# Kernel optimization log

Hardware: AMD Instinct MI355X
Metric: run time of the kernel (lower is better)

Reference implementation:

```python
import jax, jax.numpy as jnp
import numpy as np

HID = 1024
HEADS = 16
HEAD_DIM = HID // HEADS
MLP_HID = 4096
TEMB = 1024
EPS = 1e-6


def _ln(x):
    # LayerNorm without affine, eps=1e-6
    mu = jnp.mean(x, axis=-1, keepdims=True)
    var = jnp.var(x, axis=-1, keepdims=True)
    return (x - mu) * jax.lax.rsqrt(var + EPS)


def _modulate(x, shift, scale):
    return x * (1.0 + scale[:, None, :]) + shift[:, None, :]


def setup_inputs() -> dict:
    key = jax.random.key(0)
    ks = jax.random.split(key, 12)
    s = 0.02
    return {
        "x": jax.random.normal(ks[0], (8, 1024, HID), jnp.float32),
        "c": jax.random.normal(ks[1], (8, TEMB), jnp.float32),
        "W_qkv": jax.random.normal(ks[2], (HID, 3 * HID), jnp.float32) * s,
        "b_qkv": jnp.zeros((3 * HID,), jnp.float32),
        "W_proj": jax.random.normal(ks[3], (HID, HID), jnp.float32) * s,
        "b_proj": jnp.zeros((HID,), jnp.float32),
        "W_fc1": jax.random.normal(ks[4], (HID, MLP_HID), jnp.float32) * s,
        "b_fc1": jnp.zeros((MLP_HID,), jnp.float32),
        "W_fc2": jax.random.normal(ks[5], (MLP_HID, HID), jnp.float32) * s,
        "b_fc2": jnp.zeros((HID,), jnp.float32),
        "W_ada": jax.random.normal(ks[6], (TEMB, 6 * HID), jnp.float32) * s,
        "b_ada": jnp.zeros((6 * HID,), jnp.float32),
    }


def _attn(x, W_qkv, b_qkv, W_proj, b_proj):
    B, N, C = x.shape
    qkv = x @ W_qkv + b_qkv                      # [B,N,3C]
    qkv = qkv.reshape(B, N, 3, HEADS, HEAD_DIM)
    q, k, v = qkv[:, :, 0], qkv[:, :, 1], qkv[:, :, 2]  # [B,N,H,D]
    scale = HEAD_DIM ** -0.5
    logits = jnp.einsum('bnhd,bmhd->bhnm', q, k) * scale
    attn = jax.nn.softmax(logits, axis=-1)
    out = jnp.einsum('bhnm,bmhd->bnhd', attn, v).reshape(B, N, C)
    return out @ W_proj + b_proj


def reference(x, c, W_qkv, b_qkv, W_proj, b_proj, W_fc1, b_fc1, W_fc2, b_fc2, W_ada, b_ada):
    ada = jax.nn.silu(c) @ W_ada + b_ada          # [B,6C]
    shift_msa, scale_msa, gate_msa, shift_mlp, scale_mlp, gate_mlp = jnp.split(ada, 6, axis=1)

    h = _modulate(_ln(x), shift_msa, scale_msa)
    x = x + gate_msa[:, None, :] * _attn(h, W_qkv, b_qkv, W_proj, b_proj)

    h = _modulate(_ln(x), shift_mlp, scale_mlp)
    h = jax.nn.gelu(h @ W_fc1 + b_fc1, approximate=True) @ W_fc2 + b_fc2
    x = x + gate_mlp[:, None, :] * h
    return x
```

## Files before the change

### kernel.cpp

```cpp
#include <hip/hip_runtime.h>
#include <stdint.h>

typedef unsigned short u16;
typedef __attribute__((ext_vector_type(4))) float f32x4;
typedef __attribute__((ext_vector_type(8))) short bf16x8;
typedef bf16x8 bf16x8a __attribute__((may_alias));
typedef uint32_t u32a __attribute__((may_alias));

#define HID 1024
#define MLPD 4096
#define TEMB 1024
#define ADA_N 6144
#define SEQ 1024
#define BATCH 8
#define KCH 32
#define KCHLEN (TEMB / KCH)

__device__ __forceinline__ u16 f2bf_bits(float f) {
  uint32_t u = __float_as_uint(f);
  uint32_t r = (u + 0x7FFFu + ((u >> 16) & 1u)) >> 16;
  return (u16)r;
}

__device__ __forceinline__ float bf2f(u16 b) {
  return __uint_as_float(((uint32_t)b) << 16);
}

__device__ __forceinline__ uint32_t cvt_pk_bf16(float lo, float hi) {
  uint32_t r;
  asm("v_cvt_pk_bf16_f32 %0, %1, %2" : "=v"(r) : "v"(lo), "v"(hi));
  return r;
}

__device__ __forceinline__ float exp2_hw(float x) {
#if __has_builtin(__builtin_amdgcn_exp2f)
  return __builtin_amdgcn_exp2f(x);
#else
  return exp2f(x);
#endif
}

__device__ __forceinline__ void async_copy16(void* lds_dst, const void* g_src) {
  __builtin_amdgcn_global_load_lds(
      (const __attribute__((address_space(1))) void*)(uintptr_t)g_src,
      (__attribute__((address_space(3))) void*)(uint32_t)(uintptr_t)lds_dst,
      16, 0, 0);
}

__device__ __forceinline__ float gelu_tanh(float v) {
  float u = 0.7978845608028654f * (v + 0.044715f * v * v * v);
  float e = __expf(2.f * u);
  return v * e / (e + 1.f);
}

__global__ __launch_bounds__(256) void transpose_bf16(const float* __restrict__ W,
                                                      u16* __restrict__ Wt, int K, int N) {
  __shared__ float tile[32][33];
  int n0 = blockIdx.x * 32, k0 = blockIdx.y * 32;
  int tx = threadIdx.x & 31, ty = threadIdx.x >> 5;
#pragma unroll
  for (int i = 0; i < 4; i++)
    tile[ty + i * 8][tx] = W[(size_t)(k0 + ty + i * 8) * N + n0 + tx];
  __syncthreads();
#pragma unroll
  for (int i = 0; i < 4; i++)
    Wt[(size_t)(n0 + ty + i * 8) * K + k0 + tx] = f2bf_bits(tile[tx][ty + i * 8]);
}

__global__ __launch_bounds__(256) void ada_part(const float* __restrict__ c,
                                                const float* __restrict__ W,
                                                float* __restrict__ part) {
  __shared__ float sc[BATCH * KCHLEN];
  int t = threadIdx.x;
  int col = blockIdx.x * 256 + t;
  int kc = blockIdx.y;
  int k0 = kc * KCHLEN;
  for (int i = t; i < BATCH * KCHLEN; i += 256) {
    int b = i >> 5, kk = i & (KCHLEN - 1);
    float v = c[b * TEMB + k0 + kk];
    sc[i] = v / (1.f + __expf(-v));
  }
  __syncthreads();
  float acc[BATCH] = {};
  for (int kk = 0; kk < KCHLEN; kk++) {
    float w = W[(size_t)(k0 + kk) * ADA_N + col];
#pragma unroll
    for (int b = 0; b < BATCH; b++) acc[b] += sc[b * KCHLEN + kk] * w;
  }
#pragma unroll
  for (int b = 0; b < BATCH; b++)
    part[((size_t)kc * BATCH + b) * ADA_N + col] = acc[b];
}

__global__ __launch_bounds__(256) void ada_reduce(const float* __restrict__ part,
                                                  const float* __restrict__ bias,
                                                  float* __restrict__ out) {
  int i = blockIdx.x * 256 + threadIdx.x;
  int col = i % ADA_N, b = i / ADA_N;
  float s = bias[col];
#pragma unroll
  for (int kc = 0; kc < KCH; kc++)
    s += part[((size_t)kc * BATCH + b) * ADA_N + col];
  out[(size_t)b * ADA_N + col] = s;
}

__global__ __launch_bounds__(256) void ln_mod(const float* __restrict__ x,
                                              const float* __restrict__ ada,
                                              int shift_off, int scale_off,
                                              u16* __restrict__ h) {
  int row = blockIdx.x;
  int bb = row >> 10;
  int t = threadIdx.x;
  const float4 v = ((const float4*)(x + (size_t)row * HID))[t];
  float s = v.x + v.y + v.z + v.w;
  float sq = v.x * v.x + v.y * v.y + v.z * v.z + v.w * v.w;
#pragma unroll
  for (int off = 32; off >= 1; off >>= 1) {
    s += __shfl_xor(s, off);
    sq += __shfl_xor(sq, off);
  }
  __shared__ float red[8];
  int wid = t >> 6;
  if ((t & 63) == 0) { red[wid] = s; red[4 + wid] = sq; }
  __syncthreads();
  s = red[0] + red[1] + red[2] + red[3];
  sq = red[4] + red[5] + red[6] + red[7];
  float mu = s * (1.0f / HID);
  float rs = rsqrtf(sq * (1.0f / HID) - mu * mu + 1e-6f);
  const float4 sc = ((const float4*)(ada + (size_t)bb * ADA_N + scale_off))[t];
  const float4 sh = ((const float4*)(ada + (size_t)bb * ADA_N + shift_off))[t];
  ushort4 o;
  o.x = f2bf_bits((v.x - mu) * rs * (1.f + sc.x) + sh.x);
  o.y = f2bf_bits((v.y - mu) * rs * (1.f + sc.y) + sh.y);
  o.z = f2bf_bits((v.z - mu) * rs * (1.f + sc.z) + sh.z);
  o.w = f2bf_bits((v.w - mu) * rs * (1.f + sc.w) + sh.w);
  ((ushort4*)(h + (size_t)row * HID))[t] = o;
}


template <int NLOAD>
__device__ __forceinline__ void stage_tile(u16* dst, const u16* gsrc, int K, int koff, int t) {
#pragma unroll
  for (int i = 0; i < NLOAD; ++i) {
    int slot = i * 512 + t;
    int row = slot >> 3, cp = slot & 7;
    const u16* src = gsrc + (size_t)row * K + koff + ((cp ^ (row & 7)) << 3);
    async_copy16(dst + slot * 8, src);
  }
}

#define LDSRD(buf, row, kk) \
  (*(const bf16x8a*)&(buf)[(row) * 64 + ((((kk) * 4 + l4) ^ ((row) & 7)) << 3)])

template <int EPI>
__global__ __launch_bounds__(512, 2) void gemm8(const u16* __restrict__ A,
                                                const u16* __restrict__ Bt,
                                                const float* __restrict__ bias,
                                                void* __restrict__ Cout,
                                                const float* __restrict__ resid,
                                                const float* __restrict__ gate,
                                                int N, int K) {
  __shared__ u16 lds[49152];
  u16* const As0 = lds;
  u16* const As1 = lds + 16384;
  u16* const Bs0 = lds + 32768;
  u16* const Bs1 = lds + 40960;

  int t = threadIdx.x;
  int lane = t & 63, wid = t >> 6;
  int l15 = lane & 15, l4 = lane >> 4;
  int wr = wid >> 2, wc = wid & 3;
  int lid = blockIdx.x;
  int xcd = lid & 7, win = lid >> 3;
  int m0 = (xcd * 4 + (win & 3)) * 256;
  int n0 = (win >> 2) * 128;

  const u16* Abase = A + (size_t)m0 * K;
  const u16* Bbase = Bt + (size_t)n0 * K;
  f32x4 acc[8][2] = {};

  stage_tile<4>(As0, Abase, K, 0, t);
  stage_tile<2>(Bs0, Bbase, K, 0, t);
  stage_tile<4>(As1, Abase, K, 64, t);
  stage_tile<2>(Bs1, Bbase, K, 64, t);
  int nt = K / 64;
  for (int ts = 0; ts < nt; ++ts) {
    u16* cA = (ts & 1) ? As1 : As0;
    u16* cB = (ts & 1) ? Bs1 : Bs0;
    if (ts == nt - 1) asm volatile("s_waitcnt vmcnt(0)" ::: "memory");
    else              asm volatile("s_waitcnt vmcnt(6)" ::: "memory");
    __builtin_amdgcn_s_barrier();
    asm volatile("" ::: "memory");
    bf16x8 bf[2][2], af[8][2];
#pragma unroll
    for (int ni = 0; ni < 2; ++ni)
#pragma unroll
      for (int kk = 0; kk < 2; ++kk)
        bf[ni][kk] = LDSRD(cB, wc * 32 + ni * 16 + l15, kk);
#pragma unroll
    for (int mi = 0; mi < 8; ++mi)
#pragma unroll
      for (int kk = 0; kk < 2; ++kk)
        af[mi][kk] = LDSRD(cA, wr * 128 + mi * 16 + l15, kk);
    asm volatile("s_waitcnt lgkmcnt(0)" ::: "memory");
    __builtin_amdgcn_s_barrier();
    if (ts + 2 < nt) {
      stage_tile<4>(cA, Abase, K, (ts + 2) * 64, t);
      stage_tile<2>(cB, Bbase, K, (ts + 2) * 64, t);
    }
    __builtin_amdgcn_s_setprio(1);
#pragma unroll
    for (int mi = 0; mi < 8; ++mi)
#pragma unroll
      for (int ni = 0; ni < 2; ++ni) {
        acc[mi][ni] = __builtin_amdgcn_mfma_f32_16x16x32_bf16(af[mi][0], bf[ni][0], acc[mi][ni], 0, 0, 0);
        acc[mi][ni] = __builtin_amdgcn_mfma_f32_16x16x32_bf16(af[mi][1], bf[ni][1], acc[mi][ni], 0, 0, 0);
      }
    __builtin_amdgcn_s_setprio(0);
  }

  const int EST = 132;
  int bb = m0 >> 10;
#pragma unroll
  for (int ni = 0; ni < 2; ++ni) {
    int col = wc * 32 + ni * 16 + l15;
    float bv = bias[n0 + col];
    float gv = (EPI == 2) ? gate[(size_t)bb * ADA_N + n0 + col] : 0.f;
#pragma unroll
    for (int mi = 0; mi < 8; ++mi)
#pragma unroll
      for (int r = 0; r < 4; ++r) {
        int row = wr * 128 + mi * 16 + l4 * 4 + r;
        float v = acc[mi][ni][r] + bv;
        if (EPI == 1) v = gelu_tanh(v);
        if (EPI == 2) v = gv * v;
        lds[row * EST + col] = f2bf_bits(v);
      }
  }
  asm volatile("s_waitcnt lgkmcnt(0)" ::: "memory");
  __builtin_amdgcn_s_barrier();
  asm volatile("" ::: "memory");
  {
    int row = t >> 1, half = t & 1;
    size_t grow = (size_t)(m0 + row) * N + n0 + half * 64;
#pragma unroll
    for (int j = 0; j < 8; ++j) {
      bf16x8 v = *(const bf16x8a*)&lds[row * EST + half * 64 + j * 8];
      if (EPI == 2) {
        const float4* rp = (const float4*)&resid[grow + j * 8];
        float4 o0 = rp[0], o1 = rp[1];
        o0.x += bf2f((u16)v[0]); o0.y += bf2f((u16)v[1]);
        o0.z += bf2f((u16)v[2]); o0.w += bf2f((u16)v[3]);
        o1.x += bf2f((u16)v[4]); o1.y += bf2f((u16)v[5]);
        o1.z += bf2f((u16)v[6]); o1.w += bf2f((u16)v[7]);
        float4* op = (float4*)((float*)Cout + grow + j * 8);
        op[0] = o0; op[1] = o1;
      } else {
        *(bf16x8a*)((u16*)Cout + grow + j * 8) = v;
      }
    }
  }
}

__global__ __launch_bounds__(256, 3) void attn_kernel(const u16* __restrict__ qkv,
                                                      u16* __restrict__ O) {
  const int KSTR = 72, VSTR = 72, PSTR = 72;
  __shared__ u16 Ks[64 * 72];
  __shared__ u16 Vt[64 * 72];
  __shared__ u16 Plds[4 * 16 * 72];
  int t = threadIdx.x, lane = t & 63, wid = t >> 6;
  int l15 = lane & 15, l4 = lane >> 4;
  int work = ((blockIdx.x & 7) << 7) + (blockIdx.x >> 3);
  int bh = work >> 3, qt8 = work & 7;
  int b = bh >> 4, h = bh & 15;
  int bRow = b * SEQ;
  int hOff = h * 64;
  int q0 = qt8 * 128 + wid * 32;

  bf16x8 qr[2][2];
#pragma unroll
  for (int qt = 0; qt < 2; qt++) {
    const u16* qbase = qkv + (size_t)(bRow + q0 + qt * 16 + l15) * 3072 + hOff;
    qr[qt][0] = *(const bf16x8a*)(qbase + l4 * 8);
    qr[qt][1] = *(const bf16x8a*)(qbase + 32 + l4 * 8);
  }

  const float csc = 0.125f * 1.4426950408889634f;
  float mrow[2] = {-1e30f, -1e30f};
  float lsum[2] = {0.f, 0.f};
  f32x4 o[2][4] = {};
  u16* pw = Plds + wid * 16 * PSTR;

  for (int cc = 0; cc < 16; cc++) {
    int kv0 = cc * 64;
    __syncthreads();
#pragma unroll
    for (int i = 0; i < 2; i++) {
      int idx = i * 256 + t;
      int row = idx >> 3, ch = idx & 7;
      bf16x8 kk = *(const bf16x8a*)(qkv + (size_t)(bRow + kv0 + row) * 3072 + 1024 + hOff + ch * 8);
      *(bf16x8a*)&Ks[row * KSTR + ch * 8] = kk;
    }
#pragma unroll
    for (int i = 0; i < 2; i++) {
      int idx = i * 256 + t;
      int kv = idx >> 3, dc = idx & 7;
      bf16x8 vv = *(const bf16x8a*)(qkv + (size_t)(bRow + kv0 + kv) * 3072 + 2048 + hOff + dc * 8);
#pragma unroll
      for (int j = 0; j < 8; j++) {
        int jj = (j + dc) & 7;
        Vt[(dc * 8 + jj) * VSTR + kv] = ((const u16*)&vv)[jj];
      }
    }
    __syncthreads();

    bf16x8 ak[4][2];
#pragma unroll
    for (int kt = 0; kt < 4; kt++) {
      ak[kt][0] = *(const bf16x8a*)&Ks[(kt * 16 + l15) * KSTR + l4 * 8];
      ak[kt][1] = *(const bf16x8a*)&Ks[(kt * 16 + l15) * KSTR + 32 + l4 * 8];
    }
    f32x4 st[2][4];
#pragma unroll
    for (int qt = 0; qt < 2; qt++)
#pragma unroll
      for (int kt = 0; kt < 4; kt++) {
        f32x4 z = {0.f, 0.f, 0.f, 0.f};
        z = __builtin_amdgcn_mfma_f32_16x16x32_bf16(ak[kt][0], qr[qt][0], z, 0, 0, 0);
        z = __builtin_amdgcn_mfma_f32_16x16x32_bf16(ak[kt][1], qr[qt][1], z, 0, 0, 0);
        st[qt][kt] = z;
      }
    bf16x8 av[4][2];
#pragma unroll
    for (int dt = 0; dt < 4; dt++) {
      av[dt][0] = *(const bf16x8a*)&Vt[(dt * 16 + l15) * VSTR + l4 * 8];
      av[dt][1] = *(const bf16x8a*)&Vt[(dt * 16 + l15) * VSTR + 32 + l4 * 8];
    }

#pragma unroll
    for (int qt = 0; qt < 2; qt++) {
      float mx = st[qt][0][0];
#pragma unroll
      for (int kt = 0; kt < 4; kt++)
#pragma unroll
        for (int r = 0; r < 4; r++) mx = fmaxf(mx, st[qt][kt][r]);
      mx = fmaxf(mx, __shfl_xor(mx, 16));
      mx = fmaxf(mx, __shfl_xor(mx, 32));
      float mn = fmaxf(mrow[qt], mx * csc);
      float al = exp2_hw(mrow[qt] - mn);
      mrow[qt] = mn;
      float rs = 0.f;
#pragma unroll
      for (int kt = 0; kt < 4; kt++)
#pragma unroll
        for (int r = 0; r < 4; r++) {
          float p = exp2_hw(__builtin_fmaf(st[qt][kt][r], csc, -mn));
          st[qt][kt][r] = p;
          rs += p;
        }
      rs += __shfl_xor(rs, 16);
      rs += __shfl_xor(rs, 32);
      lsum[qt] = lsum[qt] * al + rs;
#pragma unroll
      for (int dt = 0; dt < 4; dt++) o[qt][dt] *= al;
#pragma unroll
      for (int kt = 0; kt < 4; kt++) {
#pragma unroll
        for (int hh = 0; hh < 2; hh++) {
          uint32_t pk = cvt_pk_bf16(st[qt][kt][2 * hh], st[qt][kt][2 * hh + 1]);
          *(u32a*)&pw[l15 * PSTR + kt * 16 + l4 * 4 + 2 * hh] = pk;
        }
      }
      asm volatile("s_waitcnt lgkmcnt(0)" ::: "memory");
      __builtin_amdgcn_sched_barrier(0);
      bf16x8 bp0 = *(const bf16x8a*)&pw[l15 * PSTR + l4 * 8];
      bf16x8 bp1 = *(const bf16x8a*)&pw[l15 * PSTR + 32 + l4 * 8];
#pragma unroll
      for (int dt = 0; dt < 4; dt++) {
        o[qt][dt] = __builtin_amdgcn_mfma_f32_16x16x32_bf16(av[dt][0], bp0, o[qt][dt], 0, 0, 0);
        o[qt][dt] = __builtin_amdgcn_mfma_f32_16x16x32_bf16(av[dt][1], bp1, o[qt][dt], 0, 0, 0);
      }
      asm volatile("s_waitcnt lgkmcnt(0)" ::: "memory");
      __builtin_amdgcn_sched_barrier(0);
    }
  }
#pragma unroll
  for (int qt = 0; qt < 2; qt++) {
    float inv = 1.f / lsum[qt];
    u16* orow = O + (size_t)(bRow + q0 + qt * 16 + l15) * HID + hOff;
#pragma unroll
    for (int dt = 0; dt < 4; dt++) {
      uint2 w;
      w.x = cvt_pk_bf16(o[qt][dt][0] * inv, o[qt][dt][1] * inv);
      w.y = cvt_pk_bf16(o[qt][dt][2] * inv, o[qt][dt][3] * inv);
      *(uint2*)(orow + dt * 16 + l4 * 4) = w;
    }
  }
}

extern "C" void kernel_launch(void* const* d_in, const int* in_sizes, int n_in,
                              void* d_out, int out_size, void* d_ws, size_t ws_size,
                              hipStream_t stream) {
  const float* x      = (const float*)d_in[0];
  const float* c      = (const float*)d_in[1];
  const float* W_qkv  = (const float*)d_in[2];
  const float* b_qkv  = (const float*)d_in[3];
  const float* W_proj = (const float*)d_in[4];
  const float* b_proj = (const float*)d_in[5];
  const float* W_fc1  = (const float*)d_in[6];
  const float* b_fc1  = (const float*)d_in[7];
  const float* W_fc2  = (const float*)d_in[8];
  const float* b_fc2  = (const float*)d_in[9];
  const float* W_ada  = (const float*)d_in[10];
  const float* b_ada  = (const float*)d_in[11];
  float* out = (float*)d_out;
  char* ws = (char*)d_ws;

  float* ada  = (float*)(ws + 0);
  u16* WtQKV  = (u16*)(ws + 196608);
  u16* WtP    = (u16*)(ws + 6488064);
  u16* WtF1   = (u16*)(ws + 8585216);
  u16* WtF2   = (u16*)(ws + 16973824);
  u16* hbuf   = (u16*)(ws + 25362432);
  u16* big    = (u16*)(ws + 42139648);
  float* apart = (float*)(ws + 42139648);

  transpose_bf16<<<dim3(3072 / 32, 1024 / 32), 256, 0, stream>>>(W_qkv, WtQKV, 1024, 3072);
  transpose_bf16<<<dim3(1024 / 32, 1024 / 32), 256, 0, stream>>>(W_proj, WtP, 1024, 1024);
  transpose_bf16<<<dim3(4096 / 32, 1024 / 32), 256, 0, stream>>>(W_fc1, WtF1, 1024, 4096);
  transpose_bf16<<<dim3(1024 / 32, 4096 / 32), 256, 0, stream>>>(W_fc2, WtF2, 4096, 1024);
  ada_part<<<dim3(ADA_N / 256, KCH), 256, 0, stream>>>(c, W_ada, apart);
  ada_reduce<<<(BATCH * ADA_N) / 256, 256, 0, stream>>>(apart, b_ada, ada);
  ln_mod<<<8192, 256, 0, stream>>>(x, ada, 0, 1024, hbuf);
  gemm8<0><<<768, 512, 0, stream>>>(hbuf, WtQKV, b_qkv, big, nullptr, nullptr, 3072, 1024);
  attn_kernel<<<1024, 256, 0, stream>>>(big, hbuf);
  gemm8<2><<<256, 512, 0, stream>>>(hbuf, WtP, b_proj, out, x, ada + 2048, 1024, 1024);
  ln_mod<<<8192, 256, 0, stream>>>(out, ada, 3072, 4096, hbuf);
  gemm8<1><<<1024, 512, 0, stream>>>(hbuf, WtF1, b_fc1, big, nullptr, nullptr, 4096, 1024);
  gemm8<2><<<256, 512, 0, stream>>>(big, WtF2, b_fc2, out, out, ada + 5120, 1024, 4096);
}
```

Baseline: 453.9 us.

## Replace 256x128 GEMM tiles with 128x128 tiles and single-step K=32 prefetch

Replaces the 512-thread GEMM, which used 256x128 tiles, K-steps of 64 and a two-deep async prefetch, with a 256-thread kernel. The new kernel uses 128x128 tiles, K-steps of 32 and a one-ahead double buffer. LDS use drops sharply and the grid doubles, so more blocks can be resident and the tail covers the CUs better. In exchange, operand reuse per loaded byte falls and there are twice as many barrier-separated K iterations. The setprio hints and the deeper load latency hiding are also dropped.

Result: faster. 429.7 us (-5.3%).

```diff
diff --git a/kernel.cpp b/kernel.cpp
--- a/kernel.cpp
+++ b/kernel.cpp
@@ -138,99 +138,88 @@
 }
 
 
-template <int NLOAD>
-__device__ __forceinline__ void stage_tile(u16* dst, const u16* gsrc, int K, int koff, int t) {
-#pragma unroll
-  for (int i = 0; i < NLOAD; ++i) {
-    int slot = i * 512 + t;
-    int row = slot >> 3, cp = slot & 7;
-    const u16* src = gsrc + (size_t)row * K + koff + ((cp ^ (row & 7)) << 3);
+__device__ __forceinline__ void stage32(u16* dst, const u16* gsrc, int K, int koff, int t) {
+#pragma unroll
+  for (int i = 0; i < 2; ++i) {
+    int slot = i * 256 + t;
+    int row = slot >> 2, cp = slot & 3;
+    const u16* src = gsrc + (size_t)row * K + koff + ((cp ^ ((row >> 1) & 3)) << 3);
     async_copy16(dst + slot * 8, src);
   }
 }
 
-#define LDSRD(buf, row, kk) \
-  (*(const bf16x8a*)&(buf)[(row) * 64 + ((((kk) * 4 + l4) ^ ((row) & 7)) << 3)])
+#define LDSRD32(buf, row) \
+  (*(const bf16x8a*)&(buf)[(row) * 32 + ((l4 ^ (((row) >> 1) & 3)) << 3)])
 
 template <int EPI>
-__global__ __launch_bounds__(512, 2) void gemm8(const u16* __restrict__ A,
-                                                const u16* __restrict__ Bt,
-                                                const float* __restrict__ bias,
-                                                void* __restrict__ Cout,
-                                                const float* __restrict__ resid,
-                                                const float* __restrict__ gate,
-                                                int N, int K) {
-  __shared__ u16 lds[49152];
+__global__ __launch_bounds__(256) void gemm2(const u16* __restrict__ A,
+                                             const u16* __restrict__ Bt,
+                                             const float* __restrict__ bias,
+                                             void* __restrict__ Cout,
+                                             const float* __restrict__ resid,
+                                             const float* __restrict__ gate,
+                                             int N, int K) {
+  __shared__ u16 lds[16896];
   u16* const As0 = lds;
-  u16* const As1 = lds + 16384;
-  u16* const Bs0 = lds + 32768;
-  u16* const Bs1 = lds + 40960;
+  u16* const As1 = lds + 4096;
+  u16* const Bs0 = lds + 8192;
+  u16* const Bs1 = lds + 12288;
 
   int t = threadIdx.x;
   int lane = t & 63, wid = t >> 6;
   int l15 = lane & 15, l4 = lane >> 4;
-  int wr = wid >> 2, wc = wid & 3;
+  int wr = wid >> 1, wc = wid & 1;
   int lid = blockIdx.x;
   int xcd = lid & 7, win = lid >> 3;
-  int m0 = (xcd * 4 + (win & 3)) * 256;
-  int n0 = (win >> 2) * 128;
+  int m0 = (xcd * 8 + (win & 7)) * 128;
+  int n0 = (win >> 3) * 128;
 
   const u16* Abase = A + (size_t)m0 * K;
   const u16* Bbase = Bt + (size_t)n0 * K;
-  f32x4 acc[8][2] = {};
-
-  stage_tile<4>(As0, Abase, K, 0, t);
-  stage_tile<2>(Bs0, Bbase, K, 0, t);
-  stage_tile<4>(As1, Abase, K, 64, t);
-  stage_tile<2>(Bs1, Bbase, K, 64, t);
-  int nt = K / 64;
+  f32x4 acc[4][4] = {};
+
+  stage32(As0, Abase, K, 0, t);
+  stage32(Bs0, Bbase, K, 0, t);
+  int nt = K / 32;
   for (int ts = 0; ts < nt; ++ts) {
     u16* cA = (ts & 1) ? As1 : As0;
     u16* cB = (ts & 1) ? Bs1 : Bs0;
-    if (ts == nt - 1) asm volatile("s_waitcnt vmcnt(0)" ::: "memory");
-    else              asm volatile("s_waitcnt vmcnt(6)" ::: "memory");
+    if (ts + 1 < nt) {
+      stage32((ts & 1) ? As0 : As1, Abase, K, (ts + 1) * 32, t);
+      stage32((ts & 1) ? Bs0 : Bs1, Bbase, K, (ts + 1) * 32, t);
+      asm volatile("s_waitcnt vmcnt(4)" ::: "memory");
+    } else {
+      asm volatile("s_waitcnt vmcnt(0)" ::: "memory");
+    }
     __builtin_amdgcn_s_barrier();
+    bf16x8 af[4], bfr[4];
+#pragma unroll
+    for (int mi = 0; mi < 4; ++mi)
+      af[mi] = LDSRD32(cA, wr * 64 + mi * 16 + l15);
+#pragma unroll
+    for (int ni = 0; ni < 4; ++ni)
+      bfr[ni] = LDSRD32(cB, wc * 64 + ni * 16 + l15);
+#pragma unroll
+    for (int mi = 0; mi < 4; ++mi)
+#pragma unroll
+      for (int ni = 0; ni < 4; ++ni)
+        acc[mi][ni] = __builtin_amdgcn_mfma_f32_16x16x32_bf16(af[mi], bfr[ni], acc[mi][ni], 0, 0, 0);
     asm volatile("" ::: "memory");
-    bf16x8 bf[2][2], af[8][2];
-#pragma unroll
-    for (int ni = 0; ni < 2; ++ni)
-#pragma unroll
-      for (int kk = 0; kk < 2; ++kk)
-        bf[ni][kk] = LDSRD(cB, wc * 32 + ni * 16 + l15, kk);
-#pragma unroll
-    for (int mi = 0; mi < 8; ++mi)
-#pragma unroll
-      for (int kk = 0; kk < 2; ++kk)
-        af[mi][kk] = LDSRD(cA, wr * 128 + mi * 16 + l15, kk);
-    asm volatile("s_waitcnt lgkmcnt(0)" ::: "memory");
     __builtin_amdgcn_s_barrier();
-    if (ts + 2 < nt) {
-      stage_tile<4>(cA, Abase, K, (ts + 2) * 64, t);
-      stage_tile<2>(cB, Bbase, K, (ts + 2) * 64, t);
-    }
-    __builtin_amdgcn_s_setprio(1);
-#pragma unroll
-    for (int mi = 0; mi < 8; ++mi)
-#pragma unroll
-      for (int ni = 0; ni < 2; ++ni) {
-        acc[mi][ni] = __builtin_amdgcn_mfma_f32_16x16x32_bf16(af[mi][0], bf[ni][0], acc[mi][ni], 0, 0, 0);
-        acc[mi][ni] = __builtin_amdgcn_mfma_f32_16x16x32_bf16(af[mi][1], bf[ni][1], acc[mi][ni], 0, 0, 0);
-      }
-    __builtin_amdgcn_s_setprio(0);
   }
 
   const int EST = 132;
   int bb = m0 >> 10;
 #pragma unroll
-  for (int ni = 0; ni < 2; ++ni) {
-    int col = wc * 32 + ni * 16 + l15;
+  for (int ni = 0; ni < 4; ++ni) {
+    int col = wc * 64 + ni * 16 + l15;
     float bv = bias[n0 + col];
     float gv = (EPI == 2) ? gate[(size_t)bb * ADA_N + n0 + col] : 0.f;
 #pragma unroll
-    for (int mi = 0; mi < 8; ++mi)
+    for (int mi = 0; mi < 4; ++mi)
 #pragma unroll
       for (int r = 0; r < 4; ++r) {
-        int row = wr * 128 + mi * 16 + l4 * 4 + r;
+        int row = wr * 64 + mi * 16 + l4 * 4 + r;
         float v = acc[mi][ni][r] + bv;
         if (EPI == 1) v = gelu_tanh(v);
         if (EPI == 2) v = gv * v;
@@ -432,10 +421,10 @@
   ada_part<<<dim3(ADA_N / 256, KCH), 256, 0, stream>>>(c, W_ada, apart);
   ada_reduce<<<(BATCH * ADA_N) / 256, 256, 0, stream>>>(apart, b_ada, ada);
   ln_mod<<<8192, 256, 0, stream>>>(x, ada, 0, 1024, hbuf);
-  gemm8<0><<<768, 512, 0, stream>>>(hbuf, WtQKV, b_qkv, big, nullptr, nullptr, 3072, 1024);
+  gemm2<0><<<1536, 256, 0, stream>>>(hbuf, WtQKV, b_qkv, big, nullptr, nullptr, 3072, 1024);
   attn_kernel<<<1024, 256, 0, stream>>>(big, hbuf);
-  gemm8<2><<<256, 512, 0, stream>>>(hbuf, WtP, b_proj, out, x, ada + 2048, 1024, 1024);
+  gemm2<2><<<512, 256, 0, stream>>>(hbuf, WtP, b_proj, out, x, ada + 2048, 1024, 1024);
   ln_mod<<<8192, 256, 0, stream>>>(out, ada, 3072, 4096, hbuf);
-  gemm8<1><<<1024, 512, 0, stream>>>(hbuf, WtF1, b_fc1, big, nullptr, nullptr, 4096, 1024);
-  gemm8<2><<<256, 512, 0, stream>>>(big, WtF2, b_fc2, out, out, ada + 5120, 1024, 4096);
-}
+  gemm2<1><<<2048, 256, 0, stream>>>(hbuf, WtF1, b_fc1, big, nullptr, nullptr, 4096, 1024);
+  gemm2<2><<<512, 256, 0, stream>>>(big, WtF2, b_fc2, out, out, ada + 5120, 1024, 4096);
+}
```
